# Kernel tuning notes

Measured on AMD Instinct MI355X. Metric: run time of the kernel, lower is better.

Reference implementation:

```python
import jax, jax.numpy as jnp
import numpy as np

K = 7  # median blur kernel size

def median_blur(x, k=K):
    # kornia.filters.median_blur: zero padding, gather kxk window per pixel,
    # torch.median -> lower median = sorted index (k*k-1)//2 (== k*k//2 for odd k*k)
    pad = k // 2
    B, C, H, W = x.shape
    xp = jnp.pad(x, ((0, 0), (0, 0), (pad, pad), (pad, pad)))
    # [B, C, k*k, H, W] patch tensor (same as kornia's unfold via binary-kernel conv)
    patches = jnp.stack(
        [xp[:, :, i:i + H, j:j + W] for i in range(k) for j in range(k)], axis=2
    )
    return jnp.sort(patches, axis=2)[:, :, (k * k) // 2]


def setup_inputs() -> dict:
    key = jax.random.key(0)
    k1, k2 = jax.random.split(key)
    image = jax.random.normal(k1, (16, 3, 256, 256), dtype=jnp.float32)
    cover_image = jax.random.normal(k2, (16, 3, 256, 256), dtype=jnp.float32)
    return {"image": image, "cover_image": cover_image}


def reference(image, cover_image):
    x = (image + 1.0) / 2.0          # [-1,1] -> [0,1]
    x = median_blur(x, K)            # 7x7 median filter (p=1.0, always applied)
    x = x * 2.0 - 1.0                # [0,1] -> [-1,1]
    return jnp.clip(x, -1.0, 1.0)
```

## Files before the change

### kernel.cpp

```cpp
#include <hip/hip_runtime.h>
#include <stdint.h>


#define IMG_H 256
#define IMG_W 256
#define RROWS 8
#define RUNS  (IMG_H / RROWS)
typedef unsigned long long u64;

#define PERM(a,b,s) __builtin_amdgcn_perm((a),(b),(s))

struct Planes6 { uint32_t pL[6], pH[6]; };

__device__ __forceinline__ Planes6 transpose6(
    uint32_t L0, uint32_t L1, uint32_t L2, uint32_t L3,
    uint32_t L4, uint32_t L5, uint32_t L6,
    uint32_t H0, uint32_t H1, uint32_t H2, uint32_t H3,
    uint32_t H4, uint32_t H5, uint32_t H6)
{
    Planes6 P;
    {
        uint32_t za1 = PERM(L1, L0, 0x05010400u), zb1 = PERM(L1, L0, 0x07030602u);
        uint32_t za2 = PERM(L3, L2, 0x05010400u), zb2 = PERM(L3, L2, 0x07030602u);
        uint32_t za3 = PERM(L5, L4, 0x05010400u), zb3 = PERM(L5, L4, 0x07030602u);
        uint32_t za4 = PERM(0u, L6, 0x05010400u), zb4 = PERM(0u, L6, 0x07030602u);
        P.pL[0] = PERM(za2, za1, 0x05040100u);  P.pH[0] = PERM(za4, za3, 0x05040100u);
        P.pL[1] = PERM(za2, za1, 0x07060302u);  P.pH[1] = PERM(za4, za3, 0x07060302u);
        P.pL[2] = PERM(zb2, zb1, 0x05040100u);  P.pH[2] = PERM(zb4, zb3, 0x05040100u);
        P.pL[3] = PERM(zb2, zb1, 0x07060302u);  P.pH[3] = PERM(zb4, zb3, 0x07060302u);
    }
    {
        uint32_t za1 = PERM(H1, H0, 0x05010400u);
        uint32_t za2 = PERM(H3, H2, 0x05010400u);
        uint32_t za3 = PERM(H5, H4, 0x05010400u);
        uint32_t za4 = PERM(0u, H6, 0x05010400u);
        P.pL[4] = PERM(za2, za1, 0x05040100u);  P.pH[4] = PERM(za4, za3, 0x05040100u);
        P.pL[5] = PERM(za2, za1, 0x07060302u);  P.pH[5] = PERM(za4, za3, 0x07060302u);
    }
    return P;
}

__device__ __forceinline__ uint32_t quant6(float v) {
    float t = fmaf(v, 31.5f, 32.0f);
    t = fminf(fmaxf(t, 0.0f), 63.0f);
    return (uint32_t)t;
}

__device__ __forceinline__ void roll2(uint32_t& lo, uint32_t& hi,
                                      uint32_t q0, uint32_t q1) {
    uint32_t n0 = ((q0 & 15u) * 0x08102040u) & 0x40404040u;
    uint32_t n1 = ((q1 & 15u) * 0x10204080u) & 0x80808080u;
    lo = ((lo >> 2) & 0x3F3F3F3Fu) | n0 | n1;
    uint32_t m0 = ((q0 >> 4) * 0x08102040u) & 0x00004040u;
    uint32_t m1 = ((q1 >> 4) * 0x10204080u) & 0x00008080u;
    hi = ((hi >> 2) & 0x00003F3Fu) | m0 | m1;
}

__device__ __forceinline__ void select2_store(
    const Planes6& P, float* __restrict__ op, int yA, int x)
{
    uint32_t acloA = 0x7F7F7F7Fu, achiA = 0x007F7F7Fu, kA = 25u, medA = 0u;
    uint32_t acloB = 0xFEFEFEFEu, achiB = 0x00FEFEFEu, kB = 25u, medB = 0u;
#pragma unroll
    for (int p = 5; p >= 1; --p) {
        {
            uint32_t ol = acloA & P.pL[p], oh = achiA & P.pH[p];
            uint32_t c1 = (uint32_t)(__popc(ol) + __popc(oh));
            bool b = (kA <= c1);
            acloA = b ? ol : (acloA ^ ol);
            achiA = b ? oh : (achiA ^ oh);
            kA    = b ? kA : (kA - c1);
            medA  = medA + medA + (b ? 1u : 0u);
        }
        {
            uint32_t ol = acloB & P.pL[p], oh = achiB & P.pH[p];
            uint32_t c1 = (uint32_t)(__popc(ol) + __popc(oh));
            bool b = (kB <= c1);
            acloB = b ? ol : (acloB ^ ol);
            achiB = b ? oh : (achiB ^ oh);
            kB    = b ? kB : (kB - c1);
            medB  = medB + medB + (b ? 1u : 0u);
        }
    }
    {
        uint32_t c1A = (uint32_t)(__popc(acloA & P.pL[0]) + __popc(achiA & P.pH[0]));
        medA = medA + medA + ((kA <= c1A) ? 1u : 0u);
        uint32_t c1B = (uint32_t)(__popc(acloB & P.pL[0]) + __popc(achiB & P.pH[0]));
        medB = medB + medB + ((kB <= c1B) ? 1u : 0u);
    }
    __builtin_nontemporal_store(fmaf((float)medA, 2.0f / 63.0f, -1.0f),
                                &op[yA * IMG_W + x]);
    __builtin_nontemporal_store(fmaf((float)medB, 2.0f / 63.0f, -1.0f),
                                &op[(yA + 1) * IMG_W + x]);
}

__global__ __launch_bounds__(256, 6)
void median7_kernel(const float* __restrict__ img, float* __restrict__ out) {
    const int x   = threadIdx.x;
    const int pl  = blockIdx.x / RUNS;
    const int run = blockIdx.x % RUNS;
    const int y0  = run * RROWS;

    const float* ip = img + (size_t)pl * (IMG_H * IMG_W);
    float*       op = out + (size_t)pl * (IMG_H * IMG_W);

    __shared__ u64 VL[2][IMG_W + 6];
    if (x < 3) {
        VL[0][x] = 0ULL; VL[1][x] = 0ULL;
        VL[0][IMG_W + 3 + x] = 0ULL; VL[1][IMG_W + 3 + x] = 0ULL;
    }

    uint32_t vlo = 0u, vhi = 0u;

    {
        float pv[6];
#pragma unroll
        for (int j = 0; j < 6; ++j) pv[j] = ip[max(y0 - 3 + j, 0) * IMG_W + x];
        uint32_t q[6];
#pragma unroll
        for (int j = 0; j < 6; ++j)
            q[j] = (y0 - 3 + j) >= 0 ? quant6(pv[j]) : 0u;
        roll2(vlo, vhi, q[0], q[1]);
        roll2(vlo, vhi, q[2], q[3]);
        roll2(vlo, vhi, q[4], q[5]);
    }
    {
        float f0 = ip[(y0 + 3) * IMG_W + x];
        float f1 = ip[(y0 + 4) * IMG_W + x];
        roll2(vlo, vhi, quant6(f0), quant6(f1));
    }
    VL[0][3 + x] = ((u64)vhi << 32) | vlo;

    float f0 = ip[min(y0 + 5, IMG_H - 1) * IMG_W + x];
    float f1 = ip[min(y0 + 6, IMG_H - 1) * IMG_W + x];

    __syncthreads();

#pragma unroll
    for (int e = 0; e < 4; ++e) {
        const u64* q = &VL[e & 1][x];
        u64 n0 = q[0], n1 = q[1], n2 = q[2], n4 = q[4], n5 = q[5], n6 = q[6];

        float nf0 = 0.0f, nf1 = 0.0f;
        if (e < 2) {
            nf0 = ip[min(y0 + 2 * e + 7, IMG_H - 1) * IMG_W + x];
            nf1 = ip[min(y0 + 2 * e + 8, IMG_H - 1) * IMG_W + x];
        }

        Planes6 P = transpose6(
            (uint32_t)n0, (uint32_t)n1, (uint32_t)n2, vlo,
            (uint32_t)n4, (uint32_t)n5, (uint32_t)n6,
            (uint32_t)(n0 >> 32), (uint32_t)(n1 >> 32), (uint32_t)(n2 >> 32), vhi,
            (uint32_t)(n4 >> 32), (uint32_t)(n5 >> 32), (uint32_t)(n6 >> 32));
        select2_store(P, op, y0 + 2 * e, x);

        if (e < 3) {
            const int ry0 = y0 + 2 * e + 5, ry1 = y0 + 2 * e + 6;
            uint32_t q0 = (ry0 < IMG_H) ? quant6(f0) : 0u;
            uint32_t q1 = (ry1 < IMG_H) ? quant6(f1) : 0u;
            roll2(vlo, vhi, q0, q1);
            VL[(e + 1) & 1][3 + x] = ((u64)vhi << 32) | vlo;
            f0 = nf0; f1 = nf1;
            __syncthreads();
        }
    }
}

extern "C" void kernel_launch(void* const* d_in, const int* in_sizes, int n_in,
                              void* d_out, int out_size, void* d_ws, size_t ws_size,
                              hipStream_t stream) {
    const float* img = (const float*)d_in[0];
    float* out = (float*)d_out;
    const int planes = in_sizes[0] / (IMG_H * IMG_W);
    dim3 grid(planes * RUNS);
    dim3 block(256);
    median7_kernel<<<grid, block, 0, stream>>>(img, out);
}
```

Before: 15.50 us.

## Batch two row-pair window states per LDS exchange to halve barriers

Each thread now computes two consecutive rolling vertical-column states and writes both into a 16-byte shared slot. Each LDS exchange and barrier therefore serves four output rows instead of two, so an 8-row run needs two barriers instead of three and uses wider shared loads. The cost is twice the shared memory per block and more live registers, since two sets of neighbour values are held at once. That could reduce occupancy.

```diff
diff --git a/kernel.cpp b/kernel.cpp
--- a/kernel.cpp
+++ b/kernel.cpp
@@ -104,10 +104,11 @@
     const float* ip = img + (size_t)pl * (IMG_H * IMG_W);
     float*       op = out + (size_t)pl * (IMG_H * IMG_W);
 
-    __shared__ u64 VL[2][IMG_W + 6];
+    __shared__ ulonglong2 VL[2][IMG_W + 6];
     if (x < 3) {
-        VL[0][x] = 0ULL; VL[1][x] = 0ULL;
-        VL[0][IMG_W + 3 + x] = 0ULL; VL[1][IMG_W + 3 + x] = 0ULL;
+        const ulonglong2 z = make_ulonglong2(0ULL, 0ULL);
+        VL[0][x] = z; VL[1][x] = z;
+        VL[0][IMG_W + 3 + x] = z; VL[1][IMG_W + 3 + x] = z;
     }
 
     uint32_t vlo = 0u, vhi = 0u;
@@ -124,45 +125,70 @@
         roll2(vlo, vhi, q[2], q[3]);
         roll2(vlo, vhi, q[4], q[5]);
     }
-    {
-        float f0 = ip[(y0 + 3) * IMG_W + x];
-        float f1 = ip[(y0 + 4) * IMG_W + x];
+    uint32_t sAlo, sAhi;
+    {
+        float f0 = ip[(y0 + 3) * IMG_W + x], f1 = ip[(y0 + 4) * IMG_W + x];
+        float f2 = ip[(y0 + 5) * IMG_W + x], f3 = ip[(y0 + 6) * IMG_W + x];
         roll2(vlo, vhi, quant6(f0), quant6(f1));
-    }
-    VL[0][3 + x] = ((u64)vhi << 32) | vlo;
-
-    float f0 = ip[min(y0 + 5, IMG_H - 1) * IMG_W + x];
-    float f1 = ip[min(y0 + 6, IMG_H - 1) * IMG_W + x];
-
+        sAlo = vlo; sAhi = vhi;
+        roll2(vlo, vhi, quant6(f2), quant6(f3));
+    }
+    VL[0][3 + x] = make_ulonglong2(((u64)sAhi << 32) | sAlo,
+                                   ((u64)vhi  << 32) | vlo);
     __syncthreads();
 
-#pragma unroll
-    for (int e = 0; e < 4; ++e) {
-        const u64* q = &VL[e & 1][x];
-        u64 n0 = q[0], n1 = q[1], n2 = q[2], n4 = q[4], n5 = q[5], n6 = q[6];
-
-        float nf0 = 0.0f, nf1 = 0.0f;
-        if (e < 2) {
-            nf0 = ip[min(y0 + 2 * e + 7, IMG_H - 1) * IMG_W + x];
-            nf1 = ip[min(y0 + 2 * e + 8, IMG_H - 1) * IMG_W + x];
-        }
-
-        Planes6 P = transpose6(
-            (uint32_t)n0, (uint32_t)n1, (uint32_t)n2, vlo,
-            (uint32_t)n4, (uint32_t)n5, (uint32_t)n6,
-            (uint32_t)(n0 >> 32), (uint32_t)(n1 >> 32), (uint32_t)(n2 >> 32), vhi,
-            (uint32_t)(n4 >> 32), (uint32_t)(n5 >> 32), (uint32_t)(n6 >> 32));
-        select2_store(P, op, y0 + 2 * e, x);
-
-        if (e < 3) {
-            const int ry0 = y0 + 2 * e + 5, ry1 = y0 + 2 * e + 6;
-            uint32_t q0 = (ry0 < IMG_H) ? quant6(f0) : 0u;
-            uint32_t q1 = (ry1 < IMG_H) ? quant6(f1) : 0u;
-            roll2(vlo, vhi, q0, q1);
-            VL[(e + 1) & 1][3 + x] = ((u64)vhi << 32) | vlo;
-            f0 = nf0; f1 = nf1;
-            __syncthreads();
-        }
+    {
+        const ulonglong2* qp = &VL[0][x];
+        ulonglong2 n0 = qp[0], n1 = qp[1], n2 = qp[2];
+        ulonglong2 n4 = qp[4], n5 = qp[5], n6 = qp[6];
+
+        float g0 = ip[(y0 + 7) * IMG_W + x];
+        float g1 = ip[min(y0 + 8,  IMG_H - 1) * IMG_W + x];
+        float g2 = ip[min(y0 + 9,  IMG_H - 1) * IMG_W + x];
+        float g3 = ip[min(y0 + 10, IMG_H - 1) * IMG_W + x];
+
+        Planes6 P0 = transpose6(
+            (uint32_t)n0.x, (uint32_t)n1.x, (uint32_t)n2.x, sAlo,
+            (uint32_t)n4.x, (uint32_t)n5.x, (uint32_t)n6.x,
+            (uint32_t)(n0.x >> 32), (uint32_t)(n1.x >> 32), (uint32_t)(n2.x >> 32), sAhi,
+            (uint32_t)(n4.x >> 32), (uint32_t)(n5.x >> 32), (uint32_t)(n6.x >> 32));
+        select2_store(P0, op, y0, x);
+
+        Planes6 P1 = transpose6(
+            (uint32_t)n0.y, (uint32_t)n1.y, (uint32_t)n2.y, vlo,
+            (uint32_t)n4.y, (uint32_t)n5.y, (uint32_t)n6.y,
+            (uint32_t)(n0.y >> 32), (uint32_t)(n1.y >> 32), (uint32_t)(n2.y >> 32), vhi,
+            (uint32_t)(n4.y >> 32), (uint32_t)(n5.y >> 32), (uint32_t)(n6.y >> 32));
+        select2_store(P1, op, y0 + 2, x);
+
+        const bool ok8 = (y0 + 8) < IMG_H, ok9 = (y0 + 9) < IMG_H,
+                   ok10 = (y0 + 10) < IMG_H;
+        roll2(vlo, vhi, quant6(g0), ok8 ? quant6(g1) : 0u);
+        sAlo = vlo; sAhi = vhi;
+        roll2(vlo, vhi, ok9 ? quant6(g2) : 0u, ok10 ? quant6(g3) : 0u);
+        VL[1][3 + x] = make_ulonglong2(((u64)sAhi << 32) | sAlo,
+                                       ((u64)vhi  << 32) | vlo);
+        __syncthreads();
+    }
+
+    {
+        const ulonglong2* qp = &VL[1][x];
+        ulonglong2 n0 = qp[0], n1 = qp[1], n2 = qp[2];
+        ulonglong2 n4 = qp[4], n5 = qp[5], n6 = qp[6];
+
+        Planes6 P0 = transpose6(
+            (uint32_t)n0.x, (uint32_t)n1.x, (uint32_t)n2.x, sAlo,
+            (uint32_t)n4.x, (uint32_t)n5.x, (uint32_t)n6.x,
+            (uint32_t)(n0.x >> 32), (uint32_t)(n1.x >> 32), (uint32_t)(n2.x >> 32), sAhi,
+            (uint32_t)(n4.x >> 32), (uint32_t)(n5.x >> 32), (uint32_t)(n6.x >> 32));
+        select2_store(P0, op, y0 + 4, x);
+
+        Planes6 P1 = transpose6(
+            (uint32_t)n0.y, (uint32_t)n1.y, (uint32_t)n2.y, vlo,
+            (uint32_t)n4.y, (uint32_t)n5.y, (uint32_t)n6.y,
+            (uint32_t)(n0.y >> 32), (uint32_t)(n1.y >> 32), (uint32_t)(n2.y >> 32), vhi,
+            (uint32_t)(n4.y >> 32), (uint32_t)(n5.y >> 32), (uint32_t)(n6.y >> 32));
+        select2_store(P1, op, y0 + 6, x);
     }
 }
 
```

Result: faster. 15.18 us (-2.0%).
